# Optimization experiments

Measured on AMD Instinct MI355X. Metric: run time of the kernel, lower is better.

## Reference

```python
import jax, jax.numpy as jnp
import numpy as np

B, S, D, H = 2, 2048, 1024, 16
DK = D // H

def setup_inputs() -> dict:
    key = jax.random.key(0)
    ks = jax.random.split(key, 12)
    scale = 1.0 / np.sqrt(D)
    return {
        "q": jax.random.normal(ks[0], (B, S, D), jnp.float32),
        "k": jax.random.normal(ks[1], (B, S, D), jnp.float32),
        "v": jax.random.normal(ks[2], (B, S, D), jnp.float32),
        "mask": jax.random.randint(ks[3], (B, 1, S, S), 0, 2, jnp.int32),
        "w_q": jax.random.normal(ks[4], (D, D), jnp.float32) * scale,
        "b_q": jnp.zeros((D,), jnp.float32),
        "w_k": jax.random.normal(ks[5], (D, D), jnp.float32) * scale,
        "b_k": jnp.zeros((D,), jnp.float32),
        "w_v": jax.random.normal(ks[6], (D, D), jnp.float32) * scale,
        "b_v": jnp.zeros((D,), jnp.float32),
        "w_o": jax.random.normal(ks[7], (D, D), jnp.float32) * scale,
        "b_o": jnp.zeros((D,), jnp.float32),
    }

def reference(q, k, v, mask, w_q, b_q, w_k, b_k, w_v, b_v, w_o, b_o):
    # projections (nn.Linear: x @ W^T + b)
    Q = q @ w_q.T + b_q  # [B,S,D]
    K = k @ w_k.T + b_k
    V = v @ w_v.T + b_v
    # split heads -> [B,H,S,DK]
    Q = Q.reshape(B, S, H, DK).transpose(0, 2, 1, 3)
    K = K.reshape(B, S, H, DK).transpose(0, 2, 1, 3)
    V = V.reshape(B, S, H, DK).transpose(0, 2, 1, 3)
    scores = jnp.einsum("bhqd,bhkd->bhqk", Q, K) / jnp.sqrt(jnp.float32(DK))
    scores = jnp.where(mask == 0, jnp.float32(-1e9), scores)
    attn = jax.nn.softmax(scores, axis=-1)  # dropout p=0 -> identity
    x = jnp.einsum("bhqk,bhkd->bhqd", attn, V)
    x = x.transpose(0, 2, 1, 3).reshape(B, S, D)
    return x @ w_o.T + b_o
```

## Files before the change

kernel.cpp:

```cpp
#include <hip/hip_runtime.h>
#include <hip/hip_bf16.h>
#include <cstdint>
#include <cstddef>

typedef short bf16x8 __attribute__((ext_vector_type(8)));
typedef short bf16x4v __attribute__((ext_vector_type(4)));
typedef float f32x4 __attribute__((ext_vector_type(4)));
typedef __hip_bfloat16 bf16;

constexpr int Bb = 2, Ss = 2048, Dd = 1024, Hh = 16, DKk = 64;

__device__ __forceinline__ void async_lds16(void* lds, const void* g) {
  __builtin_amdgcn_global_load_lds(
      (const __attribute__((address_space(1))) void*)g,
      (__attribute__((address_space(3))) void*)lds, 16, 0, 0);
}

__device__ __forceinline__ float bf2f(bf16 x) { return __bfloat162float(x); }
__device__ __forceinline__ short f2bf(float x) {
  bf16 h = __float2bfloat16(x);
  return *(short*)&h;
}
__device__ __forceinline__ short f2bf_fast(float x) {
  return (short)((__float_as_uint(x) + 0x8000u) >> 16);
}
__device__ __forceinline__ uint32_t pack2bf(float a, float b) {
  return ((__float_as_uint(a) + 0x8000u) >> 16) |
         ((__float_as_uint(b) + 0x8000u) & 0xffff0000u);
}
__device__ __forceinline__ float bfs2f(short s) {
  return __uint_as_float(((uint32_t)(uint16_t)s) << 16);
}

struct CvtArgs {
  const float* src[12];
  short* dst[12];
  int n[12];
  int count;
};

__global__ __launch_bounds__(256)
void cvt_all(CvtArgs a, const int* __restrict__ mask, uint32_t* __restrict__ bits)
{
  const int t = blockIdx.y;
  if (t == 11) {
    const int stride = 1024 * 256;
    int i = blockIdx.x * 256 + threadIdx.x;
#pragma unroll 4
    for (int it = 0; it < 32; ++it, i += stride) {
      const unsigned long long bal = __ballot(mask[i] != 0);
      if ((threadIdx.x & 63) == 0)
        *(unsigned long long*)(bits + (i >> 5)) = bal;
    }
    return;
  }
  if (t >= a.count) return;
  const float* s = a.src[t];
  short* d = a.dst[t];
  const int n = a.n[t];
  const int stride = gridDim.x * blockDim.x * 4;
  for (int i = (blockIdx.x * blockDim.x + threadIdx.x) * 4; i < n; i += stride) {
    const float4 v = *(const float4*)(s + i);
    bf16x4v o;
    o[0] = f2bf(v.x); o[1] = f2bf(v.y); o[2] = f2bf(v.z); o[3] = f2bf(v.w);
    *(bf16x4v*)(d + i) = o;
  }
}

__global__ __launch_bounds__(256, 3)
void gemm_bt(const bf16* __restrict__ A0, const bf16* __restrict__ A1, const bf16* __restrict__ A2,
             const bf16* __restrict__ W0, const bf16* __restrict__ W1, const bf16* __restrict__ W2,
             const bf16* __restrict__ b0, const bf16* __restrict__ b1, const bf16* __restrict__ b2,
             void* __restrict__ O0, void* __restrict__ O1, void* __restrict__ O2,
             float scale0, int vtrans)
{
  extern __shared__ char smem[];
  const int mt  = blockIdx.x;
  const int by  = blockIdx.y;
  const int mat = by >> 3;
  const int nt  = by & 7;
  const bf16* A    = (mat == 0) ? A0 : (mat == 1) ? A1 : A2;
  const bf16* W    = (mat == 0) ? W0 : (mat == 1) ? W1 : W2;
  const bf16* bias = (mat == 0) ? b0 : (mat == 1) ? b1 : b2;
  void*       Out  = (mat == 0) ? O0 : (mat == 1) ? O1 : O2;
  const float scale = (mat == 0) ? scale0 : 1.0f;

  const int tid  = threadIdx.x;
  const int w    = tid >> 6;
  const int lane = tid & 63;
  const int quad = lane >> 4;
  const int l16  = lane & 15;
  const int wm   = (w & 1) * 64;
  const int wn   = (w >> 1) * 64;

  const int srow = lane >> 3;
  const int sseg = (lane & 7) ^ srow;

  const char* Abytes = (const char*)A;
  const char* Wbytes = (const char*)W;

  f32x4 acc[4][4];
#pragma unroll
  for (int i = 0; i < 4; ++i)
#pragma unroll
    for (int j = 0; j < 4; ++j) acc[i][j] = f32x4{0.f, 0.f, 0.f, 0.f};

  for (int kt = 0; kt < 16; ++kt) {
    __syncthreads();
#pragma unroll
    for (int c = 0; c < 4; ++c) {
      const int r0 = w * 32 + c * 8;
      async_lds16(smem + r0 * 128,
                  Abytes + (size_t)(mt * 128 + r0 + srow) * 2048 + kt * 128 + sseg * 16);
      async_lds16(smem + 16384 + r0 * 128,
                  Wbytes + (size_t)(nt * 128 + r0 + srow) * 2048 + kt * 128 + sseg * 16);
    }
    __syncthreads();
#pragma unroll
    for (int s = 0; s < 2; ++s) {
      bf16x8 af[4], bfg[4];
#pragma unroll
      for (int mb = 0; mb < 4; ++mb) {
        const int row = wm + mb * 16 + l16;
        af[mb] = *(const bf16x8*)(smem + row * 128 + (((4 * s + quad) ^ (row & 7)) * 16));
      }
#pragma unroll
      for (int nb = 0; nb < 4; ++nb) {
        const int row = wn + nb * 16 + l16;
        bfg[nb] = *(const bf16x8*)(smem + 16384 + row * 128 + (((4 * s + quad) ^ (row & 7)) * 16));
      }
#pragma unroll
      for (int mb = 0; mb < 4; ++mb)
#pragma unroll
        for (int nb = 0; nb < 4; ++nb)
          acc[mb][nb] = __builtin_amdgcn_mfma_f32_16x16x32_bf16(af[mb], bfg[nb], acc[mb][nb], 0, 0, 0);
    }
  }

  if (vtrans && mat == 2) {
    __syncthreads();
#pragma unroll
    for (int nb = 0; nb < 4; ++nb) {
      const int dk = wn + nb * 16 + l16;
      const float bv = bf2f(bias[nt * 128 + dk]);
#pragma unroll
      for (int mb = 0; mb < 4; ++mb) {
        const int s0 = wm + mb * 16 + quad * 4;
        bf16x4v pk;
#pragma unroll
        for (int r = 0; r < 4; ++r) pk[r] = f2bf_fast(acc[mb][nb][r] + bv);
        *(bf16x4v*)(smem + dk * 256 + (((s0 >> 3) ^ (dk & 15)) * 16) + (s0 & 7) * 2) = pk;
      }
    }
    __syncthreads();
    const int bidx  = (mt * 128) >> 11;
    const int sbase = (mt * 128) & 2047;
#pragma unroll
    for (int i = 0; i < 8; ++i) {
      const int dk  = i * 16 + (tid >> 4);
      const int seg = tid & 15;
      bf16x8 vrow = *(const bf16x8*)(smem + dk * 256 + ((seg ^ (dk & 15)) * 16));
      *(bf16x8*)((bf16*)Out + (size_t)bidx * 2097152 + (size_t)(nt * 128 + dk) * 2048
                 + sbase + seg * 8) = vrow;
    }
  } else {
#pragma unroll
    for (int nb = 0; nb < 4; ++nb) {
      const int col = nt * 128 + wn + nb * 16 + l16;
      const float bv = bf2f(bias[col]);
#pragma unroll
      for (int mb = 0; mb < 4; ++mb) {
#pragma unroll
        for (int r = 0; r < 4; ++r) {
          const int row = mt * 128 + wm + mb * 16 + quad * 4 + r;
          short s = f2bf_fast((acc[mb][nb][r] + bv) * scale);
          ((short*)Out)[(size_t)row * 1024 + col] = s;
        }
      }
    }
  }
}

__global__ __launch_bounds__(256, 4)
void gemm_out(const bf16* __restrict__ A, const bf16* __restrict__ W,
              const bf16* __restrict__ bias, float* __restrict__ Out)
{
  __shared__ char smem[16384];
  const int mt = blockIdx.x;
  const int nt = blockIdx.y;
  const int tid = threadIdx.x, w = tid >> 6, lane = tid & 63;
  const int quad = lane >> 4, l16 = lane & 15;
  const int wm = (w & 1) * 32, wn = (w >> 1) * 32;
  const int srow = lane >> 3;
  const int sseg = (lane & 7) ^ (srow & 7);

  const char* Abytes = (const char*)A;
  const char* Wbytes = (const char*)W;

  f32x4 acc[2][2];
#pragma unroll
  for (int i = 0; i < 2; ++i)
#pragma unroll
    for (int j = 0; j < 2; ++j) acc[i][j] = f32x4{0.f, 0.f, 0.f, 0.f};

  for (int kt = 0; kt < 16; ++kt) {
    __syncthreads();
#pragma unroll
    for (int c = 0; c < 2; ++c) {
      const int r0 = c * 32 + w * 8;
      async_lds16(smem + c * 4096 + w * 1024,
                  Abytes + (size_t)(mt * 64 + r0 + srow) * 2048 + kt * 128 + sseg * 16);
      async_lds16(smem + 8192 + c * 4096 + w * 1024,
                  Wbytes + (size_t)(nt * 64 + r0 + srow) * 2048 + kt * 128 + sseg * 16);
    }
    __syncthreads();
#pragma unroll
    for (int s = 0; s < 2; ++s) {
      bf16x8 af[2], bfg[2];
#pragma unroll
      for (int mb = 0; mb < 2; ++mb) {
        const int row = wm + mb * 16 + l16;
        af[mb] = *(const bf16x8*)(smem + row * 128 + (((4 * s + quad) ^ (row & 7)) * 16));
      }
#pragma unroll
      for (int nb = 0; nb < 2; ++nb) {
        const int row = wn + nb * 16 + l16;
        bfg[nb] = *(const bf16x8*)(smem + 8192 + row * 128 + (((4 * s + quad) ^ (row & 7)) * 16));
      }
#pragma unroll
      for (int mb = 0; mb < 2; ++mb)
#pragma unroll
        for (int nb = 0; nb < 2; ++nb)
          acc[mb][nb] = __builtin_amdgcn_mfma_f32_16x16x32_bf16(af[mb], bfg[nb], acc[mb][nb], 0, 0, 0);
    }
  }

#pragma unroll
  for (int nb = 0; nb < 2; ++nb) {
    const int col = nt * 64 + wn + nb * 16 + l16;
    const float bv = bf2f(bias[col]);
#pragma unroll
    for (int mb = 0; mb < 2; ++mb) {
#pragma unroll
      for (int r = 0; r < 4; ++r) {
        const int row = mt * 64 + wm + mb * 16 + quad * 4 + r;
        Out[(size_t)row * 1024 + col] = acc[mb][nb][r] + bv;
      }
    }
  }
}

__global__ __launch_bounds__(256, 3)
void attn(const bf16* __restrict__ Qp, const bf16* __restrict__ Kp,
          const bf16* __restrict__ VpT, const uint32_t* __restrict__ mbits,
          bf16* __restrict__ Opart, float* __restrict__ Lpart)
{
  __shared__ char smem[49152];
  char* Kb = smem;
  char* Vt = smem + 16384;
  char* Ph = smem + 32768;

  const int tile  = blockIdx.x;
  const int split = blockIdx.y;
  const int qt = tile & 15, h = (tile >> 4) & 15, b = tile >> 8;
  const int tid = threadIdx.x, w = tid >> 6, lane = tid & 63;
  const int quad = lane >> 4, l16 = lane & 15;
  const int qb = qt * 128;
  const size_t headoff = (size_t)b * (Ss * Dd) + h * DKk;

  const int kc0 = (split == 0) ? 0 : (split == 1) ? 6 : 11;
  const int kc1 = (split == 0) ? 6 : (split == 1) ? 11 : 16;

  bf16x8 qf[2][2];
#pragma unroll
  for (int set = 0; set < 2; ++set)
#pragma unroll
    for (int s2 = 0; s2 < 2; ++s2) {
      const int row = qb + w * 32 + set * 16 + l16;
      qf[set][s2] = *(const bf16x8*)(Qp + headoff + (size_t)row * Dd + s2 * 32 + quad * 8);
    }

  f32x4 o[2][4];
  float Lacc[2] = {0.f, 0.f};
#pragma unroll
  for (int set = 0; set < 2; ++set)
#pragma unroll
    for (int nbk = 0; nbk < 4; ++nbk) o[set][nbk] = f32x4{0.f, 0.f, 0.f, 0.f};

  const uint32_t* mrow0 = mbits + (size_t)(b * Ss + qb + w * 32 + l16) * 64;
  const uint32_t* mrow1 = mrow0 + 16 * 64;

  char* Preg = (w < 2) ? smem : Ph;
  const int prowbase = (w & 1) * 32;

  for (int kc = kc0; kc < kc1; ++kc) {
    const int kb = kc * 128;
    __syncthreads();
#pragma unroll
    for (int c = 0; c < 4; ++c) {
      {
        const int row = c * 32 + w * 8 + (lane >> 3);
        const int seg = (lane & 7) ^ (row & 7);
        async_lds16(Kb + c * 4096 + w * 1024,
                    Kp + headoff + (size_t)(kb + row) * Dd + seg * 8);
      }
      {
        const int row = c * 16 + w * 4 + (lane >> 4);
        const int seg = (lane & 15) ^ (row & 15);
        async_lds16(Vt + c * 4096 + w * 1024,
                    VpT + (size_t)b * 2097152 + (size_t)(h * 64 + row) * 2048 + kb + seg * 8);
      }
    }
    __syncthreads();

    f32x4 sc[2][8];
#pragma unroll
    for (int set = 0; set < 2; ++set)
#pragma unroll
      for (int nb = 0; nb < 8; ++nb) sc[set][nb] = f32x4{0.f, 0.f, 0.f, 0.f};
#pragma unroll
    for (int s2 = 0; s2 < 2; ++s2)
#pragma unroll
      for (int nb = 0; nb < 8; ++nb) {
        const int row = nb * 16 + l16;
        bf16x8 kf = *(const bf16x8*)(Kb + row * 128 + (((s2 * 4 + quad) ^ (row & 7)) * 16));
        sc[0][nb] = __builtin_amdgcn_mfma_f32_16x16x32_bf16(kf, qf[0][s2], sc[0][nb], 0, 0, 0);
        sc[1][nb] = __builtin_amdgcn_mfma_f32_16x16x32_bf16(kf, qf[1][s2], sc[1][nb], 0, 0, 0);
      }
    __syncthreads();

#pragma unroll
    for (int set = 0; set < 2; ++set) {
      const uint4 mwv = *(const uint4*)((set == 0 ? mrow0 : mrow1) + kc * 4);
      const uint32_t mwa[4] = {mwv.x, mwv.y, mwv.z, mwv.w};
      char* Prow = Preg + (size_t)(prowbase + set * 16 + l16) * 256;
#pragma unroll
      for (int nb = 0; nb < 8; ++nb) {
        const uint32_t nib = (mwa[nb >> 1] >> ((nb & 1) * 16 + quad * 4)) & 0xFu;
        const float p0 = (nib & 1u) ? __expf(sc[set][nb][0]) : 0.f;
        const float p1 = (nib & 2u) ? __expf(sc[set][nb][1]) : 0.f;
        const float p2 = (nib & 4u) ? __expf(sc[set][nb][2]) : 0.f;
        const float p3 = (nib & 8u) ? __expf(sc[set][nb][3]) : 0.f;
        Lacc[set] += (p0 + p1) + (p2 + p3);
        uint2 pk;
        pk.x = pack2bf(p0, p1);
        pk.y = pack2bf(p2, p3);
        *(uint2*)(Prow + (((2 * nb + (quad >> 1)) ^ l16) * 16) + (quad & 1) * 8) = pk;
      }
    }
    asm volatile("s_waitcnt lgkmcnt(0)" ::: "memory");

#pragma unroll
    for (int kb4 = 0; kb4 < 2; ++kb4)
#pragma unroll
      for (int u = 0; u < 2; ++u) {
        bf16x8 pf[2];
#pragma unroll
        for (int set = 0; set < 2; ++set)
          pf[set] = *(const bf16x8*)(Preg + (size_t)(prowbase + set * 16 + l16) * 256 +
                                     (((kb4 * 8 + u * 4 + quad) ^ l16) * 16));
#pragma unroll
        for (int nbk = 0; nbk < 4; ++nbk) {
          const int row = nbk * 16 + l16;
          bf16x8 vf = *(const bf16x8*)(Vt + row * 256 +
                                       (((kb4 * 8 + u * 4 + quad) ^ (row & 15)) * 16));
          o[0][nbk] = __builtin_amdgcn_mfma_f32_16x16x32_bf16(pf[0], vf, o[0][nbk], 0, 0, 0);
          o[1][nbk] = __builtin_amdgcn_mfma_f32_16x16x32_bf16(pf[1], vf, o[1][nbk], 0, 0, 0);
        }
      }
  }

#pragma unroll
  for (int set = 0; set < 2; ++set) {
    float Lq = Lacc[set];
    Lq += __shfl_xor(Lq, 16);
    Lq += __shfl_xor(Lq, 32);
    const int rbase = tile * 128 + w * 32 + set * 16;
#pragma unroll
    for (int r = 0; r < 4; ++r) {
      const int rglob = rbase + quad * 4 + r;
#pragma unroll
      for (int nbk = 0; nbk < 4; ++nbk) {
        short s = f2bf_fast(o[set][nbk][r]);
        ((short*)Opart)[((size_t)split * 65536 + rglob) * 64 + nbk * 16 + l16] = s;
      }
    }
    if (quad == 0)
      Lpart[(size_t)split * 65536 + rbase + l16] = Lq;
  }
}

__global__ __launch_bounds__(256)
void combine(const bf16* __restrict__ Opart, const float* __restrict__ Lpart,
             bf16* __restrict__ Xa)
{
  const int t = threadIdx.x;
  const int row = blockIdx.x * 32 + (t >> 3);
  const int dkc = (t & 7) * 8;
  const float L = Lpart[row] + Lpart[65536 + row] + Lpart[131072 + row];
  const float inv = 1.0f / L;
  const bf16x8 O0 = *(const bf16x8*)(Opart + (size_t)row * 64 + dkc);
  const bf16x8 O1 = *(const bf16x8*)(Opart + ((size_t)65536 + row) * 64 + dkc);
  const bf16x8 O2 = *(const bf16x8*)(Opart + ((size_t)131072 + row) * 64 + dkc);
  bf16x8 res;
#pragma unroll
  for (int j = 0; j < 8; ++j)
    res[j] = f2bf_fast((bfs2f(O0[j]) + bfs2f(O1[j]) + bfs2f(O2[j])) * inv);
  const int tile = row >> 7, qlocal = row & 127;
  const int b = tile >> 8, h = (tile >> 4) & 15, q = (tile & 15) * 128 + qlocal;
  *(bf16x8*)(Xa + (size_t)(b * 2048 + q) * 1024 + h * 64 + dkc) = res;
}

extern "C" void kernel_launch(void* const* d_in, const int* in_sizes, int n_in,
                              void* d_out, int out_size, void* d_ws, size_t ws_size,
                              hipStream_t stream)
{
  const float* q  = (const float*)d_in[0];
  const float* k  = (const float*)d_in[1];
  const float* v  = (const float*)d_in[2];
  const int*   mk = (const int*)d_in[3];
  const float* wq = (const float*)d_in[4];
  const float* bq = (const float*)d_in[5];
  const float* wk = (const float*)d_in[6];
  const float* bk = (const float*)d_in[7];
  const float* wv = (const float*)d_in[8];
  const float* bv = (const float*)d_in[9];
  const float* wo = (const float*)d_in[10];
  const float* bo = (const float*)d_in[11];
  float* out = (float*)d_out;

  char* ws = (char*)d_ws;
  bf16* qb_  = (bf16*)(ws + ((size_t)0  << 20));
  bf16* kb_  = (bf16*)(ws + ((size_t)8  << 20));
  bf16* vb_  = (bf16*)(ws + ((size_t)16 << 20));
  bf16* Qp   = (bf16*)(ws + ((size_t)24 << 20));
  bf16* Kp   = (bf16*)(ws + ((size_t)32 << 20));
  bf16* VpT  = (bf16*)(ws + ((size_t)40 << 20));
  bf16* wqb  = (bf16*)(ws + ((size_t)48 << 20));
  bf16* wkb  = (bf16*)(ws + ((size_t)50 << 20));
  bf16* wvb  = (bf16*)(ws + ((size_t)52 << 20));
  bf16* wob  = (bf16*)(ws + ((size_t)54 << 20));
  bf16* bqb  = (bf16*)(ws + ((size_t)56 << 20));
  bf16* bkb  = (bf16*)(ws + ((size_t)56 << 20) + 2048);
  bf16* bvb  = (bf16*)(ws + ((size_t)56 << 20) + 4096);
  bf16* bob  = (bf16*)(ws + ((size_t)56 << 20) + 6144);
  uint32_t* mbits = (uint32_t*)(ws + ((size_t)56 << 20) + 65536);
  bf16*  Opart = (bf16*)(ws + ((size_t)0 << 20));
  float* Lpart = (float*)(ws + ((size_t)48 << 20));
  bf16*  Xa    = (bf16*)(ws + ((size_t)24 << 20));

  const int NA = Bb * Ss * Dd;
  const int NW = Dd * Dd;

  CvtArgs ca;
  ca.src[0] = q;  ca.dst[0] = (short*)qb_; ca.n[0] = NA;
  ca.src[1] = k;  ca.dst[1] = (short*)kb_; ca.n[1] = NA;
  ca.src[2] = v;  ca.dst[2] = (short*)vb_; ca.n[2] = NA;
  ca.src[3] = wq; ca.dst[3] = (short*)wqb; ca.n[3] = NW;
  ca.src[4] = wk; ca.dst[4] = (short*)wkb; ca.n[4] = NW;
  ca.src[5] = wv; ca.dst[5] = (short*)wvb; ca.n[5] = NW;
  ca.src[6] = wo; ca.dst[6] = (short*)wob; ca.n[6] = NW;
  ca.src[7] = bq; ca.dst[7] = (short*)bqb; ca.n[7] = Dd;
  ca.src[8] = bk; ca.dst[8] = (short*)bkb; ca.n[8] = Dd;
  ca.src[9] = bv; ca.dst[9] = (short*)bvb; ca.n[9] = Dd;
  ca.src[10] = bo; ca.dst[10] = (short*)bob; ca.n[10] = Dd;
  ca.src[11] = bo; ca.dst[11] = (short*)bob; ca.n[11] = 0;
  ca.count = 11;

  dim3 blk(256);
  cvt_all<<<dim3(1024, 12), blk, 0, stream>>>(ca, mk, mbits);

  gemm_bt<<<dim3(32, 24), blk, 32768, stream>>>(qb_, kb_, vb_, wqb, wkb, wvb,
                                                bqb, bkb, bvb,
                                                (void*)Qp, (void*)Kp, (void*)VpT,
                                                0.125f, 1);
  attn<<<dim3(512, 3), blk, 0, stream>>>(Qp, Kp, VpT, mbits, Opart, Lpart);
  combine<<<dim3(2048), blk, 0, stream>>>(Opart, Lpart, Xa);
  gemm_out<<<dim3(64, 16), blk, 0, stream>>>(Xa, wob, bob, out);
}
```

Measured before the change: 276.6 us.

## Keep attention probabilities in registers via permlane swaps instead of LDS round-trip

The attention kernel now computes QK^T in 32-key slices and rearranges the bf16 probability fragments between lanes with permlane32/permlane16 swaps, feeding them straight into the PV MFMA. This removes the LDS staging buffer for P, along with a barrier and an lgkmcnt wait per chunk. LDS use drops from 48KB to 32KB, so occupancy is raised to 4 blocks. The exponent now uses exp2 with log2(e) folded into the Q projection scale, and the float-to-bf16 packing uses the hardware v_cvt_pk_bf16_f32 instruction. The risk is higher register pressure under the tighter launch bound, and less instruction-level parallelism from the smaller per-slice MFMA batches.

```diff
diff --git a/kernel.cpp b/kernel.cpp
--- a/kernel.cpp
+++ b/kernel.cpp
@@ -6,6 +6,7 @@
 typedef short bf16x8 __attribute__((ext_vector_type(8)));
 typedef short bf16x4v __attribute__((ext_vector_type(4)));
 typedef float f32x4 __attribute__((ext_vector_type(4)));
+typedef unsigned int uint32x2 __attribute__((ext_vector_type(2)));
 typedef __hip_bfloat16 bf16;
 
 constexpr int Bb = 2, Ss = 2048, Dd = 1024, Hh = 16, DKk = 64;
@@ -24,12 +25,19 @@
 __device__ __forceinline__ short f2bf_fast(float x) {
   return (short)((__float_as_uint(x) + 0x8000u) >> 16);
 }
-__device__ __forceinline__ uint32_t pack2bf(float a, float b) {
-  return ((__float_as_uint(a) + 0x8000u) >> 16) |
-         ((__float_as_uint(b) + 0x8000u) & 0xffff0000u);
-}
 __device__ __forceinline__ float bfs2f(short s) {
   return __uint_as_float(((uint32_t)(uint16_t)s) << 16);
+}
+__device__ __forceinline__ uint32_t cvtpk_bf16(float lo, float hi) {
+  uint32_t r;
+  asm("v_cvt_pk_bf16_f32 %0, %1, %2" : "=v"(r) : "v"(lo), "v"(hi));
+  return r;
+}
+__device__ __forceinline__ uint32x2 pl32swap(uint32_t d, uint32_t s) {
+  return __builtin_amdgcn_permlane32_swap(d, s, false, false);
+}
+__device__ __forceinline__ uint32x2 pl16swap(uint32_t d, uint32_t s) {
+  return __builtin_amdgcn_permlane16_swap(d, s, false, false);
 }
 
 struct CvtArgs {
@@ -250,15 +258,14 @@
   }
 }
 
-__global__ __launch_bounds__(256, 3)
+__global__ __launch_bounds__(256, 4)
 void attn(const bf16* __restrict__ Qp, const bf16* __restrict__ Kp,
           const bf16* __restrict__ VpT, const uint32_t* __restrict__ mbits,
           bf16* __restrict__ Opart, float* __restrict__ Lpart)
 {
-  __shared__ char smem[49152];
+  __shared__ char smem[32768];
   char* Kb = smem;
   char* Vt = smem + 16384;
-  char* Ph = smem + 32768;
 
   const int tile  = blockIdx.x;
   const int split = blockIdx.y;
@@ -290,9 +297,6 @@
   const uint32_t* mrow0 = mbits + (size_t)(b * Ss + qb + w * 32 + l16) * 64;
   const uint32_t* mrow1 = mrow0 + 16 * 64;
 
-  char* Preg = (w < 2) ? smem : Ph;
-  const int prowbase = (w & 1) * 32;
-
   for (int kc = kc0; kc < kc1; ++kc) {
     const int kb = kc * 128;
     __syncthreads();
@@ -313,61 +317,67 @@
     }
     __syncthreads();
 
-    f32x4 sc[2][8];
-#pragma unroll
-    for (int set = 0; set < 2; ++set)
-#pragma unroll
-      for (int nb = 0; nb < 8; ++nb) sc[set][nb] = f32x4{0.f, 0.f, 0.f, 0.f};
-#pragma unroll
-    for (int s2 = 0; s2 < 2; ++s2)
-#pragma unroll
-      for (int nb = 0; nb < 8; ++nb) {
-        const int row = nb * 16 + l16;
-        bf16x8 kf = *(const bf16x8*)(Kb + row * 128 + (((s2 * 4 + quad) ^ (row & 7)) * 16));
-        sc[0][nb] = __builtin_amdgcn_mfma_f32_16x16x32_bf16(kf, qf[0][s2], sc[0][nb], 0, 0, 0);
-        sc[1][nb] = __builtin_amdgcn_mfma_f32_16x16x32_bf16(kf, qf[1][s2], sc[1][nb], 0, 0, 0);
-      }
-    __syncthreads();
-
-#pragma unroll
-    for (int set = 0; set < 2; ++set) {
-      const uint4 mwv = *(const uint4*)((set == 0 ? mrow0 : mrow1) + kc * 4);
-      const uint32_t mwa[4] = {mwv.x, mwv.y, mwv.z, mwv.w};
-      char* Prow = Preg + (size_t)(prowbase + set * 16 + l16) * 256;
-#pragma unroll
-      for (int nb = 0; nb < 8; ++nb) {
-        const uint32_t nib = (mwa[nb >> 1] >> ((nb & 1) * 16 + quad * 4)) & 0xFu;
-        const float p0 = (nib & 1u) ? __expf(sc[set][nb][0]) : 0.f;
-        const float p1 = (nib & 2u) ? __expf(sc[set][nb][1]) : 0.f;
-        const float p2 = (nib & 4u) ? __expf(sc[set][nb][2]) : 0.f;
-        const float p3 = (nib & 8u) ? __expf(sc[set][nb][3]) : 0.f;
-        Lacc[set] += (p0 + p1) + (p2 + p3);
-        uint2 pk;
-        pk.x = pack2bf(p0, p1);
-        pk.y = pack2bf(p2, p3);
-        *(uint2*)(Prow + (((2 * nb + (quad >> 1)) ^ l16) * 16) + (quad & 1) * 8) = pk;
-      }
-    }
-    asm volatile("s_waitcnt lgkmcnt(0)" ::: "memory");
-
-#pragma unroll
-    for (int kb4 = 0; kb4 < 2; ++kb4)
-#pragma unroll
-      for (int u = 0; u < 2; ++u) {
-        bf16x8 pf[2];
-#pragma unroll
-        for (int set = 0; set < 2; ++set)
-          pf[set] = *(const bf16x8*)(Preg + (size_t)(prowbase + set * 16 + l16) * 256 +
-                                     (((kb4 * 8 + u * 4 + quad) ^ l16) * 16));
-#pragma unroll
-        for (int nbk = 0; nbk < 4; ++nbk) {
-          const int row = nbk * 16 + l16;
-          bf16x8 vf = *(const bf16x8*)(Vt + row * 256 +
-                                       (((kb4 * 8 + u * 4 + quad) ^ (row & 15)) * 16));
-          o[0][nbk] = __builtin_amdgcn_mfma_f32_16x16x32_bf16(pf[0], vf, o[0][nbk], 0, 0, 0);
-          o[1][nbk] = __builtin_amdgcn_mfma_f32_16x16x32_bf16(pf[1], vf, o[1][nbk], 0, 0, 0);
+    const uint4 mwv0 = *(const uint4*)(mrow0 + kc * 4);
+    const uint4 mwv1 = *(const uint4*)(mrow1 + kc * 4);
+    const uint32_t mw0[4] = {mwv0.x, mwv0.y, mwv0.z, mwv0.w};
+    const uint32_t mw1[4] = {mwv1.x, mwv1.y, mwv1.z, mwv1.w};
+
+#pragma unroll
+    for (int sl = 0; sl < 4; ++sl) {
+      f32x4 sc[2][2];
+#pragma unroll
+      for (int set = 0; set < 2; ++set)
+#pragma unroll
+        for (int nbh = 0; nbh < 2; ++nbh) sc[set][nbh] = f32x4{0.f, 0.f, 0.f, 0.f};
+#pragma unroll
+      for (int s2 = 0; s2 < 2; ++s2)
+#pragma unroll
+        for (int nbh = 0; nbh < 2; ++nbh) {
+          const int row = (sl * 2 + nbh) * 16 + l16;
+          bf16x8 kf = *(const bf16x8*)(Kb + row * 128 + (((s2 * 4 + quad) ^ (row & 7)) * 16));
+          sc[0][nbh] = __builtin_amdgcn_mfma_f32_16x16x32_bf16(kf, qf[0][s2], sc[0][nbh], 0, 0, 0);
+          sc[1][nbh] = __builtin_amdgcn_mfma_f32_16x16x32_bf16(kf, qf[1][s2], sc[1][nbh], 0, 0, 0);
         }
-      }
+
+      bf16x8 pf[2];
+#pragma unroll
+      for (int set = 0; set < 2; ++set) {
+        const uint32_t mword = (set == 0) ? mw0[sl] : mw1[sl];
+        uint32_t pk[2][2];
+        float Ls = 0.f;
+#pragma unroll
+        for (int nbh = 0; nbh < 2; ++nbh) {
+          const uint32_t nib = (mword >> (nbh * 16 + quad * 4)) & 0xFu;
+          const float e0 = __builtin_amdgcn_exp2f(sc[set][nbh][0]);
+          const float e1 = __builtin_amdgcn_exp2f(sc[set][nbh][1]);
+          const float e2 = __builtin_amdgcn_exp2f(sc[set][nbh][2]);
+          const float e3 = __builtin_amdgcn_exp2f(sc[set][nbh][3]);
+          const float p0 = (nib & 1u) ? e0 : 0.f;
+          const float p1 = (nib & 2u) ? e1 : 0.f;
+          const float p2 = (nib & 4u) ? e2 : 0.f;
+          const float p3 = (nib & 8u) ? e3 : 0.f;
+          Ls += (p0 + p1) + (p2 + p3);
+          pk[nbh][0] = cvtpk_bf16(p0, p1);
+          pk[nbh][1] = cvtpk_bf16(p2, p3);
+        }
+        Lacc[set] += Ls;
+        const uint32x2 r0 = pl32swap(pk[0][0], pk[1][0]);
+        const uint32x2 r1 = pl32swap(pk[0][1], pk[1][1]);
+        const uint32x2 t0 = pl16swap(r0.x, r0.y);
+        const uint32x2 t1 = pl16swap(r1.x, r1.y);
+        union { uint32_t u[4]; bf16x8 v; } U;
+        U.u[0] = t0.x; U.u[1] = t1.x; U.u[2] = t0.y; U.u[3] = t1.y;
+        pf[set] = U.v;
+      }
+
+#pragma unroll
+      for (int nbk = 0; nbk < 4; ++nbk) {
+        const int row = nbk * 16 + l16;
+        bf16x8 vf = *(const bf16x8*)(Vt + row * 256 + (((sl * 4 + quad) ^ (row & 15)) * 16));
+        o[0][nbk] = __builtin_amdgcn_mfma_f32_16x16x32_bf16(pf[0], vf, o[0][nbk], 0, 0, 0);
+        o[1][nbk] = __builtin_amdgcn_mfma_f32_16x16x32_bf16(pf[1], vf, o[1][nbk], 0, 0, 0);
+      }
+    }
   }
 
 #pragma unroll
@@ -473,7 +483,7 @@
   gemm_bt<<<dim3(32, 24), blk, 32768, stream>>>(qb_, kb_, vb_, wqb, wkb, wvb,
                                                 bqb, bkb, bvb,
                                                 (void*)Qp, (void*)Kp, (void*)VpT,
-                                                0.125f, 1);
+                                                0.125f * 1.44269504088896340736f, 1);
   attn<<<dim3(512, 3), blk, 0, stream>>>(Qp, Kp, VpT, mbits, Opart, Lpart);
   combine<<<dim3(2048), blk, 0, stream>>>(Opart, Lpart, Xa);
   gemm_out<<<dim3(64, 16), blk, 0, stream>>>(Xa, wob, bob, out);
```

New measurement: 264.4 us. -4.4%, faster.
